# Kernel tuning notes

Measured on AMD Instinct MI355X. Metric: run time of the kernel, lower is better.

## Reference

```python
import jax, jax.numpy as jnp
import numpy as np

EPS_ATTN = 1e-6
LN_EPS = 1e-5

def _layernorm(x, g, b):
    mu = jnp.mean(x, axis=-1, keepdims=True)
    var = jnp.var(x, axis=-1, keepdims=True)
    return (x - mu) * jax.lax.rsqrt(var + LN_EPS) * g + b

def _phi(x):
    return jax.nn.elu(x) + 1.0

def setup_inputs() -> dict:
    key = jax.random.key(0)
    ks = jax.random.split(key, 8)
    B, T, D, H = 2, 4096, 128, 128  # D = token_dim = d+1, H = hidden_dim
    s = 0.02
    return {
        "tokens": jax.random.normal(ks[0], (B, T, D), dtype=jnp.float32),
        "Wq": jax.random.normal(ks[1], (D, H), dtype=jnp.float32) * s,
        "Wk": jax.random.normal(ks[2], (D, H), dtype=jnp.float32) * s,
        "Wv": jax.random.normal(ks[3], (D, D), dtype=jnp.float32) * s,
        "Wg": jax.random.normal(ks[4], (D, D), dtype=jnp.float32) * s,
        "bg": jnp.zeros((D,), dtype=jnp.float32),
        "Wo": jax.random.normal(ks[5], (D, D), dtype=jnp.float32) * s,
        "g1": jnp.ones((D,), dtype=jnp.float32),
        "b1": jnp.zeros((D,), dtype=jnp.float32),
        "g2": jnp.ones((D,), dtype=jnp.float32),
        "b2": jnp.zeros((D,), dtype=jnp.float32),
    }

def reference(tokens, Wq, Wk, Wv, Wg, bg, Wo, g1, b1, g2, b2):
    x = _layernorm(tokens, g1, b1)                 # (b,t,m)
    Q = x @ Wq                                     # (b,t,h)
    K = x @ Wk                                     # (b,t,h)
    V = x @ Wv                                     # (b,t,m)
    G = jax.nn.sigmoid(x @ Wg + bg)                # (b,t,m)
    Vg = V * G
    Qp = _phi(Q)
    Kp = _phi(K)
    # causal linear attention via cumulative outer products
    kv = jnp.einsum('bth,btm->bthm', Kp, Vg)       # (b,t,h,m)
    S_kv = jnp.cumsum(kv, axis=1)
    S_k = jnp.cumsum(Kp, axis=1)
    numerator = jnp.einsum('bth,bthm->btm', Qp, S_kv)
    denom = jnp.maximum(jnp.einsum('bth,bth->bt', Qp, S_k), EPS_ATTN)
    attn_out = numerator / denom[..., None]
    out = tokens + (attn_out @ Wo) * 0.1
    return _layernorm(out, g2, b2)
```

## Files before the change

### kernel.cpp

```cpp
#include <hip/hip_runtime.h>
#include <math.h>

#define T_ 4096
#define D_ 128
#define NTOK 8192
#define CHUNK 64
#define NCB 64
#define NCH 128
#define LN_EPS 1e-5f
#define EPS_ATTN 1e-6f

typedef __attribute__((ext_vector_type(8))) short bf16x8;
typedef __attribute__((ext_vector_type(4))) short bf16x4;
typedef __attribute__((ext_vector_type(4))) float f32x4;

__device__ inline short f2bf(float f) {
  unsigned u = __builtin_bit_cast(unsigned, f);
  u += 0x7fffu + ((u >> 16) & 1u);
  return (short)(u >> 16);
}
__device__ inline float bf2f(short s) {
  unsigned u = ((unsigned)(unsigned short)s) << 16;
  return __builtin_bit_cast(float, u);
}
__device__ inline float phi_(float x) { return x > 0.f ? x + 1.f : __expf(x); }

__global__ __launch_bounds__(256) void k_qkvg(const float* __restrict__ tokens,
    const float* __restrict__ Wq, const float* __restrict__ Wk,
    const float* __restrict__ Wv, const float* __restrict__ Wg,
    const float* __restrict__ g1, const float* __restrict__ b1,
    const float* __restrict__ bg,
    short* __restrict__ Qp, short* __restrict__ Kp, short* __restrict__ KpT,
    short* __restrict__ VgT) {
  const int m0 = blockIdx.x * 64;
  const int y = blockIdx.y;
  const int tid = threadIdx.x;
  const int w = tid >> 6, l = tid & 63;
  __shared__ short xs[64][136];
  __shared__ short wsd[128][136];

  {
    const int half = l >> 5;
    const int c4 = (l & 31) * 4;
    float4 tv[8];
    #pragma unroll
    for (int it = 0; it < 8; ++it) {
      const int t = m0 + w*16 + it*2 + half;
      tv[it] = *(const float4*)&tokens[t*D_ + c4];
    }
    const float4 gg = *(const float4*)&g1[c4];
    const float4 bb = *(const float4*)&b1[c4];
    #pragma unroll
    for (int it = 0; it < 8; ++it) {
      const float4 v = tv[it];
      float s = v.x+v.y+v.z+v.w;
      float q = v.x*v.x+v.y*v.y+v.z*v.z+v.w*v.w;
      #pragma unroll
      for (int off = 1; off < 32; off <<= 1) {
        s += __shfl_xor(s, off); q += __shfl_xor(q, off);
      }
      const float mean = s*(1.f/D_);
      const float r = rsqrtf(q*(1.f/D_) - mean*mean + LN_EPS);
      bf16x4 o;
      o.x = f2bf((v.x-mean)*r*gg.x + bb.x);
      o.y = f2bf((v.y-mean)*r*gg.y + bb.y);
      o.z = f2bf((v.z-mean)*r*gg.z + bb.z);
      o.w = f2bf((v.w-mean)*r*gg.w + bb.w);
      *(bf16x4*)&xs[w*16 + it*2 + half][c4] = o;
    }
  }

  auto stageW = [&](const float* __restrict__ W) {
    #pragma unroll
    for (int it = 0; it < 16; ++it) {
      const int f = it*1024 + tid*4;
      const int k = f >> 7, n = f & 127;
      const float4 v = *(const float4*)&W[f];
      wsd[n  ][k] = f2bf(v.x);
      wsd[n+1][k] = f2bf(v.y);
      wsd[n+2][k] = f2bf(v.z);
      wsd[n+3][k] = f2bf(v.w);
    }
  };

  const int i = l & 15, q = l >> 4;
  auto gemm = [&](f32x4 (*acc)[2]) {
    #pragma unroll
    for (int kk = 0; kk < 4; ++kk) {
      bf16x8 a[4], bfr[2];
      #pragma unroll
      for (int mt = 0; mt < 4; ++mt) a[mt] = *(const bf16x8*)&xs[mt*16+i][kk*32+q*8];
      #pragma unroll
      for (int nt = 0; nt < 2; ++nt) bfr[nt] = *(const bf16x8*)&wsd[w*32+nt*16+i][kk*32+q*8];
      #pragma unroll
      for (int mt = 0; mt < 4; ++mt)
        #pragma unroll
        for (int nt = 0; nt < 2; ++nt)
          acc[mt][nt] = __builtin_amdgcn_mfma_f32_16x16x32_bf16(a[mt], bfr[nt], acc[mt][nt], 0, 0, 0);
    }
  };

  stageW(y == 0 ? Wq : (y == 1 ? Wk : Wv));
  __syncthreads();
  f32x4 acc[4][2];
  #pragma unroll
  for (int mt = 0; mt < 4; ++mt)
    #pragma unroll
    for (int nt = 0; nt < 2; ++nt) acc[mt][nt] = (f32x4){0.f,0.f,0.f,0.f};
  gemm(acc);

  if (y == 0) {
    #pragma unroll
    for (int mt = 0; mt < 4; ++mt)
      #pragma unroll
      for (int nt = 0; nt < 2; ++nt) {
        const int h = w*32 + nt*16 + i;
        #pragma unroll
        for (int r = 0; r < 4; ++r)
          Qp[(m0 + mt*16 + 4*q + r)*D_ + h] = f2bf(phi_(acc[mt][nt][r]));
      }
  } else if (y == 1) {
    #pragma unroll
    for (int mt = 0; mt < 4; ++mt)
      #pragma unroll
      for (int nt = 0; nt < 2; ++nt) {
        const int h = w*32 + nt*16 + i;
        const int t0 = m0 + mt*16 + 4*q;
        bf16x4 o;
        #pragma unroll
        for (int r = 0; r < 4; ++r) {
          const short bv = f2bf(phi_(acc[mt][nt][r]));
          Kp[(t0+r)*D_ + h] = bv;
          o[r] = bv;
        }
        *(bf16x4*)&KpT[h*NTOK + t0] = o;
      }
  } else {
    __syncthreads();
    stageW(Wg);
    __syncthreads();
    f32x4 accg[4][2];
    #pragma unroll
    for (int mt = 0; mt < 4; ++mt)
      #pragma unroll
      for (int nt = 0; nt < 2; ++nt) accg[mt][nt] = (f32x4){0.f,0.f,0.f,0.f};
    gemm(accg);
    #pragma unroll
    for (int mt = 0; mt < 4; ++mt)
      #pragma unroll
      for (int nt = 0; nt < 2; ++nt) {
        const int h = w*32 + nt*16 + i;
        const int t0 = m0 + mt*16 + 4*q;
        const float bgd = bg[h];
        bf16x4 o;
        #pragma unroll
        for (int r = 0; r < 4; ++r) {
          const float gv = 1.f/(1.f + __expf(-(accg[mt][nt][r] + bgd)));
          o[r] = f2bf(acc[mt][nt][r] * gv);
        }
        *(bf16x4*)&VgT[h*NTOK + t0] = o;
      }
  }
}

__global__ __launch_bounds__(256) void k_chunkkv(const short* __restrict__ KpT,
    const short* __restrict__ VgT,
    float* __restrict__ KVT, float* __restrict__ Ksum) {
  const int c = blockIdx.x, hh = blockIdx.y;
  const int tid = threadIdx.x;
  const int tb = c*CHUNK;
  __shared__ short vgl[128][72];
  __shared__ short kpl[64][72];
  __shared__ float ksp[64][5];
  #pragma unroll
  for (int u = tid; u < 1024; u += 256) {
    const int d = u >> 3, c8 = (u & 7)*8;
    *(bf16x8*)&vgl[d][c8] = *(const bf16x8*)&VgT[d*NTOK + tb + c8];
  }
  #pragma unroll
  for (int u = tid; u < 512; u += 256) {
    const int h = u >> 3, c8 = (u & 7)*8;
    *(bf16x8*)&kpl[h][c8] = *(const bf16x8*)&KpT[(hh*64+h)*NTOK + tb + c8];
  }
  __syncthreads();
  const int w = tid >> 6, l = tid & 63, i = l & 15, q = l >> 4;
  f32x4 acc[2][4];
  #pragma unroll
  for (int mt = 0; mt < 2; ++mt)
    #pragma unroll
    for (int nt = 0; nt < 4; ++nt) acc[mt][nt] = (f32x4){0.f,0.f,0.f,0.f};
  #pragma unroll
  for (int kk = 0; kk < 2; ++kk) {
    bf16x8 a[2], bb[4];
    #pragma unroll
    for (int mt = 0; mt < 2; ++mt) a[mt] = *(const bf16x8*)&vgl[(2*w+mt)*16+i][kk*32+q*8];
    #pragma unroll
    for (int nt = 0; nt < 4; ++nt) bb[nt] = *(const bf16x8*)&kpl[nt*16+i][kk*32+q*8];
    #pragma unroll
    for (int mt = 0; mt < 2; ++mt)
      #pragma unroll
      for (int nt = 0; nt < 4; ++nt)
        acc[mt][nt] = __builtin_amdgcn_mfma_f32_16x16x32_bf16(a[mt], bb[nt], acc[mt][nt], 0, 0, 0);
  }
  float* KVc = KVT + (size_t)c*16384;
  #pragma unroll
  for (int mt = 0; mt < 2; ++mt)
    #pragma unroll
    for (int nt = 0; nt < 4; ++nt)
      #pragma unroll
      for (int r = 0; r < 4; ++r) {
        const int d = (2*w+mt)*16 + 4*q + r;
        const int h = hh*64 + nt*16 + i;
        KVc[d*128 + h] = acc[mt][nt][r];
      }
  {
    const int h = tid >> 2, part = tid & 3;
    float s = 0.f;
    #pragma unroll
    for (int t = 0; t < 16; ++t) s += bf2f(kpl[h][part*16 + t]);
    ksp[h][part] = s;
  }
  __syncthreads();
  if (tid < 64)
    Ksum[c*128 + hh*64 + tid] = ksp[tid][0]+ksp[tid][1]+ksp[tid][2]+ksp[tid][3];
}

__global__ __launch_bounds__(256) void k_prescore(const float* __restrict__ KVT,
    short* __restrict__ KVTb, float* __restrict__ Ksum,
    const short* __restrict__ Qp, const short* __restrict__ Kp,
    short* __restrict__ A, float* __restrict__ rowsum) {
  const int tid = threadIdx.x;
  if (blockIdx.x < 128) {
    const int b = blockIdx.x >> 6;
    const int e = (blockIdx.x & 63)*256 + tid;
    const size_t base = (size_t)b*NCB*16384 + e;
    float run = 0.f;
    #pragma unroll 8
    for (int c = 0; c < NCB; ++c) {
      const float v = KVT[base + (size_t)c*16384];
      KVTb[base + (size_t)c*16384] = f2bf(run);
      run += v;
    }
    return;
  }
  if (blockIdx.x == 128) {
    const int b = tid >> 7, h = tid & 127;
    float run = 0.f;
    #pragma unroll 8
    for (int c = 0; c < NCB; ++c) {
      const int idx = (b*NCB + c)*128 + h;
      const float v = Ksum[idx];
      Ksum[idx] = run;
      run += v;
    }
    return;
  }
  const int c = blockIdx.x - 129;
  const int tb = c*CHUNK;
  __shared__ short qpl[64][136], kpl[64][136];
  #pragma unroll
  for (int u = tid; u < 1024; u += 256) {
    const int t = u >> 4, c8 = (u & 15)*8;
    *(bf16x8*)&qpl[t][c8] = *(const bf16x8*)&Qp[(tb+t)*D_ + c8];
    *(bf16x8*)&kpl[t][c8] = *(const bf16x8*)&Kp[(tb+t)*D_ + c8];
  }
  __syncthreads();
  const int w = tid >> 6, l = tid & 63, i = l & 15, q = l >> 4;
  f32x4 acc[4];
  #pragma unroll
  for (int nt = 0; nt < 4; ++nt) acc[nt] = (f32x4){0.f,0.f,0.f,0.f};
  #pragma unroll
  for (int kk = 0; kk < 4; ++kk) {
    bf16x8 a = *(const bf16x8*)&qpl[w*16+i][kk*32+q*8];
    for (int nt = 0; nt <= w; ++nt) {
      bf16x8 bb = *(const bf16x8*)&kpl[nt*16+i][kk*32+q*8];
      acc[nt] = __builtin_amdgcn_mfma_f32_16x16x32_bf16(a, bb, acc[nt], 0, 0, 0);
    }
  }
  short* Ac = A + c*4096;
  float rs[4] = {0.f,0.f,0.f,0.f};
  #pragma unroll
  for (int nt = 0; nt < 4; ++nt) {
    #pragma unroll
    for (int r = 0; r < 4; ++r) {
      const int t = w*16 + 4*q + r;
      const int s = nt*16 + i;
      const float v = (nt <= w && s <= t) ? acc[nt][r] : 0.f;
      rs[r] += v;
      Ac[t*64 + s] = f2bf(v);
    }
  }
  #pragma unroll
  for (int r = 0; r < 4; ++r) {
    #pragma unroll
    for (int off = 1; off < 16; off <<= 1) rs[r] += __shfl_xor(rs[r], off);
  }
  if (i == 0) {
    #pragma unroll
    for (int r = 0; r < 4; ++r) rowsum[c*64 + w*16 + 4*q + r] = rs[r];
  }
}

__global__ __launch_bounds__(256) void k_attnout(const short* __restrict__ Aintra,
    const short* __restrict__ Qp, const short* __restrict__ VgT,
    const short* __restrict__ KVTb, const float* __restrict__ Ksum,
    const float* __restrict__ rowsum, short* __restrict__ attn) {
  const int c = blockIdx.x, dh = blockIdx.y, tid = threadIdx.x;
  const int tb = c*CHUNK;
  __shared__ short at[64][200], bt[64][200];
  __shared__ float ksl[128], dpart[64][4], denl[64];
  const short* Ac = Aintra + c*4096;
  #pragma unroll
  for (int u = tid; u < 512; u += 256) {
    const int t = u >> 3, c8 = (u & 7)*8;
    *(bf16x8*)&at[t][c8] = *(const bf16x8*)&Ac[t*64 + c8];
  }
  #pragma unroll
  for (int u = tid; u < 1024; u += 256) {
    const int t = u >> 4, c8 = (u & 15)*8;
    *(bf16x8*)&at[t][64 + c8] = *(const bf16x8*)&Qp[(tb+t)*D_ + c8];
  }
  #pragma unroll
  for (int u = tid; u < 512; u += 256) {
    const int dd = u >> 3, c8 = (u & 7)*8;
    *(bf16x8*)&bt[dd][c8] = *(const bf16x8*)&VgT[(dh*64+dd)*NTOK + tb + c8];
  }
  #pragma unroll
  for (int u = tid; u < 1024; u += 256) {
    const int dd = u >> 4, c8 = (u & 15)*8;
    *(bf16x8*)&bt[dd][64 + c8] = *(const bf16x8*)&KVTb[(size_t)c*16384 + (dh*64+dd)*128 + c8];
  }
  if (tid < 128) ksl[tid] = Ksum[c*128 + tid];
  __syncthreads();
  {
    const int t = tid >> 2, part = tid & 3;
    float dot = 0.f;
    #pragma unroll
    for (int h = 0; h < 32; ++h) dot += bf2f(at[t][64 + part*32 + h]) * ksl[part*32 + h];
    dpart[t][part] = dot;
  }
  __syncthreads();
  if (tid < 64)
    denl[tid] = fmaxf(rowsum[c*64 + tid] + dpart[tid][0]+dpart[tid][1]+dpart[tid][2]+dpart[tid][3], EPS_ATTN);
  __syncthreads();
  const int w = tid >> 6, l = tid & 63, i = l & 15, q = l >> 4;
  f32x4 acc[4];
  #pragma unroll
  for (int nt = 0; nt < 4; ++nt) acc[nt] = (f32x4){0.f,0.f,0.f,0.f};
  #pragma unroll
  for (int kk = 0; kk < 6; ++kk) {
    bf16x8 a = *(const bf16x8*)&at[w*16+i][kk*32+q*8];
    #pragma unroll
    for (int nt = 0; nt < 4; ++nt) {
      bf16x8 bb = *(const bf16x8*)&bt[nt*16+i][kk*32+q*8];
      acc[nt] = __builtin_amdgcn_mfma_f32_16x16x32_bf16(a, bb, acc[nt], 0, 0, 0);
    }
  }
  #pragma unroll
  for (int r = 0; r < 4; ++r) {
    const int t = w*16 + 4*q + r;
    const float inv = 1.f / denl[t];
    #pragma unroll
    for (int nt = 0; nt < 4; ++nt)
      attn[(size_t)(tb+t)*D_ + dh*64 + nt*16 + i] = f2bf(acc[nt][r] * inv);
  }
}

__global__ __launch_bounds__(256) void k_outln2(const short* __restrict__ attn,
    const float* __restrict__ Wo, const float* __restrict__ tokens,
    const float* __restrict__ g2, const float* __restrict__ b2,
    float* __restrict__ out) {
  const int m0 = blockIdx.x*32, tid = threadIdx.x;
  __shared__ short al[32][136], wl[128][136];
  __shared__ float tl[32][132];
  __shared__ float suml[32][2], ssql[32][2];
  __shared__ float meanl[32], rstdl[32];
  __shared__ float gl[128], bl2[128];
  #pragma unroll
  for (int u = tid; u < 512; u += 256) {
    const int t = u >> 4, c8 = (u & 15)*8;
    *(bf16x8*)&al[t][c8] = *(const bf16x8*)&attn[(m0+t)*D_ + c8];
  }
  #pragma unroll
  for (int it = 0; it < 16; ++it) {
    const int f = it*1024 + tid*4;
    const int k = f >> 7, n = f & 127;
    const float4 v = *(const float4*)&Wo[f];
    wl[n  ][k] = f2bf(v.x);
    wl[n+1][k] = f2bf(v.y);
    wl[n+2][k] = f2bf(v.z);
    wl[n+3][k] = f2bf(v.w);
  }
  #pragma unroll
  for (int u = tid; u < 1024; u += 256) {
    const int t = u >> 5, c4 = (u & 31)*4;
    *(float4*)&tl[t][c4] = *(const float4*)&tokens[(m0+t)*D_ + c4];
  }
  if (tid < 128) { gl[tid] = g2[tid]; bl2[tid] = b2[tid]; }
  __syncthreads();
  const int w = tid >> 6, l = tid & 63, i = l & 15, q = l >> 4;
  const int mt = w >> 1, nh = w & 1;
  f32x4 acc[4];
  #pragma unroll
  for (int j = 0; j < 4; ++j) acc[j] = (f32x4){0.f,0.f,0.f,0.f};
  #pragma unroll
  for (int kk = 0; kk < 4; ++kk) {
    bf16x8 a = *(const bf16x8*)&al[mt*16+i][kk*32+q*8];
    #pragma unroll
    for (int j = 0; j < 4; ++j) {
      bf16x8 bb = *(const bf16x8*)&wl[(nh*4+j)*16+i][kk*32+q*8];
      acc[j] = __builtin_amdgcn_mfma_f32_16x16x32_bf16(a, bb, acc[j], 0, 0, 0);
    }
  }
  float p[4][4], ps[4], qs[4];
  #pragma unroll
  for (int r = 0; r < 4; ++r) {
    const int t = mt*16 + 4*q + r;
    ps[r] = 0.f; qs[r] = 0.f;
    #pragma unroll
    for (int j = 0; j < 4; ++j) {
      const int col = nh*64 + j*16 + i;
      const float v = tl[t][col] + 0.1f*acc[j][r];
      p[r][j] = v; ps[r] += v; qs[r] += v*v;
    }
  }
  #pragma unroll
  for (int r = 0; r < 4; ++r) {
    #pragma unroll
    for (int off = 1; off < 16; off <<= 1) {
      ps[r] += __shfl_xor(ps[r], off);
      qs[r] += __shfl_xor(qs[r], off);
    }
  }
  if (i == 0) {
    #pragma unroll
    for (int r = 0; r < 4; ++r) {
      suml[mt*16+4*q+r][nh] = ps[r];
      ssql[mt*16+4*q+r][nh] = qs[r];
    }
  }
  __syncthreads();
  if (tid < 32) {
    const float s = suml[tid][0] + suml[tid][1];
    const float qq = ssql[tid][0] + ssql[tid][1];
    const float mean = s*(1.f/D_);
    meanl[tid] = mean;
    rstdl[tid] = rsqrtf(qq*(1.f/D_) - mean*mean + LN_EPS);
  }
  __syncthreads();
  #pragma unroll
  for (int r = 0; r < 4; ++r) {
    const int t = mt*16 + 4*q + r;
    const float mean = meanl[t], rr = rstdl[t];
    #pragma unroll
    for (int j = 0; j < 4; ++j) {
      const int col = nh*64 + j*16 + i;
      out[(m0+t)*D_ + col] = (p[r][j]-mean)*rr*gl[col] + bl2[col];
    }
  }
}

extern "C" void kernel_launch(void* const* d_in, const int* in_sizes, int n_in,
                              void* d_out, int out_size, void* d_ws, size_t ws_size,
                              hipStream_t stream) {
  const float* tokens = (const float*)d_in[0];
  const float* Wq = (const float*)d_in[1];
  const float* Wk = (const float*)d_in[2];
  const float* Wv = (const float*)d_in[3];
  const float* Wg = (const float*)d_in[4];
  const float* bg = (const float*)d_in[5];
  const float* Wo = (const float*)d_in[6];
  const float* g1 = (const float*)d_in[7];
  const float* b1 = (const float*)d_in[8];
  const float* g2 = (const float*)d_in[9];
  const float* b2 = (const float*)d_in[10];

  char* base = (char*)d_ws;
  short* Qp     = (short*)(base);
  short* Kp     = (short*)(base + (2u<<20));
  short* KpT    = (short*)(base + (4u<<20));
  short* VgT    = (short*)(base + (6u<<20));
  short* attn   = (short*)(base + (8u<<20));
  short* KVTb   = (short*)(base + (10u<<20));
  short* Aintra = (short*)(base + (14u<<20));
  float* rowsum = (float*)(base + (15u<<20));
  float* Ksum   = (float*)(base + (15u<<20) + (256u<<10));
  float* KVT    = (float*)(base + (16u<<20));

  k_qkvg<<<dim3(NTOK/64, 3), 256, 0, stream>>>(tokens, Wq, Wk, Wv, Wg, g1, b1, bg,
                                               Qp, Kp, KpT, VgT);
  k_chunkkv<<<dim3(NCH, 2), 256, 0, stream>>>(KpT, VgT, KVT, Ksum);
  k_prescore<<<257, 256, 0, stream>>>(KVT, KVTb, Ksum, Qp, Kp, Aintra, rowsum);
  k_attnout<<<dim3(NCH, 2), 256, 0, stream>>>(Aintra, Qp, VgT, KVTb, Ksum, rowsum, attn);
  k_outln2<<<NTOK/32, 256, 0, stream>>>(attn, Wo, tokens, g2, b2, (float*)d_out);
}
```

Measured before the change: 120.3 us.

## Fuse pipeline into persistent megakernel with grid barriers

Replaces the five separate kernel launches with one persistent kernel of 256 blocks that runs each stage in a grid-stride loop, separated by atomic-counter grid barriers. It also pre-transposes and converts the weights to bf16 once, and materializes the layernormed input in bf16. The scan and prescore stages are reorganized, so the chunk-prefix pass and the intra-chunk scoring now run as separate barrier phases. The aim is to remove launch gaps and redundant per-block weight conversion, at the cost of spin-wait barriers, a memset launch, and reliance on all 256 blocks being co-resident.

```diff
diff --git a/kernel.cpp b/kernel.cpp
--- a/kernel.cpp
+++ b/kernel.cpp
@@ -7,6 +7,7 @@
 #define CHUNK 64
 #define NCB 64
 #define NCH 128
+#define NBLK 256
 #define LN_EPS 1e-5f
 #define EPS_ATTN 1e-6f
 
@@ -25,437 +26,463 @@
 }
 __device__ inline float phi_(float x) { return x > 0.f ? x + 1.f : __expf(x); }
 
-__global__ __launch_bounds__(256) void k_qkvg(const float* __restrict__ tokens,
-    const float* __restrict__ Wq, const float* __restrict__ Wk,
-    const float* __restrict__ Wv, const float* __restrict__ Wg,
-    const float* __restrict__ g1, const float* __restrict__ b1,
-    const float* __restrict__ bg,
-    short* __restrict__ Qp, short* __restrict__ Kp, short* __restrict__ KpT,
-    short* __restrict__ VgT) {
-  const int m0 = blockIdx.x * 64;
-  const int y = blockIdx.y;
+__device__ inline void gbar(unsigned* cnt) {
+  __syncthreads();
+  if (threadIdx.x == 0) {
+    __threadfence();
+    atomicAdd(cnt, 1u);
+    while (atomicAdd(cnt, 0u) < NBLK) __builtin_amdgcn_s_sleep(1);
+    __threadfence();
+  }
+  __syncthreads();
+}
+
+struct Params {
+  const float *tokens, *Wq, *Wk, *Wv, *Wg, *bg, *Wo, *g1, *b1, *g2, *b2;
+  short *xb, *WT, *Qp, *Kp, *KpT, *VgT, *attn, *KVTb;
+  float *KVT, *Ksum, *out;
+  unsigned *bar;
+};
+
+struct S0 { float tile[32][33]; };
+struct S1 { short xs[64][136]; short wsd[128][136]; };
+struct S2 { short vgl[128][72]; short kpl[64][72]; float ksp[64][5]; };
+struct S4 { short at[64][200]; short bt[64][200];
+            float ksl[128]; float rsl[64]; float dpart[64][4]; float denl[64]; };
+struct S5 { short al[32][136]; short wl[128][136]; float tl[32][132];
+            float suml[32][2]; float ssql[32][2]; float meanl[32]; float rstdl[32];
+            float gl[128]; float bl2[128]; };
+
+__global__ __launch_bounds__(256, 1) void mega(Params P) {
+  __shared__ union { S0 s0; S1 s1; S2 s2; S4 s4; S5 s5; } sm;
   const int tid = threadIdx.x;
-  const int w = tid >> 6, l = tid & 63;
-  __shared__ short xs[64][136];
-  __shared__ short wsd[128][136];
-
-  {
-    const int half = l >> 5;
-    const int c4 = (l & 31) * 4;
-    float4 tv[8];
-    #pragma unroll
-    for (int it = 0; it < 8; ++it) {
-      const int t = m0 + w*16 + it*2 + half;
-      tv[it] = *(const float4*)&tokens[t*D_ + c4];
-    }
-    const float4 gg = *(const float4*)&g1[c4];
-    const float4 bb = *(const float4*)&b1[c4];
-    #pragma unroll
-    for (int it = 0; it < 8; ++it) {
-      const float4 v = tv[it];
-      float s = v.x+v.y+v.z+v.w;
-      float q = v.x*v.x+v.y*v.y+v.z*v.z+v.w*v.w;
-      #pragma unroll
-      for (int off = 1; off < 32; off <<= 1) {
-        s += __shfl_xor(s, off); q += __shfl_xor(q, off);
-      }
-      const float mean = s*(1.f/D_);
-      const float r = rsqrtf(q*(1.f/D_) - mean*mean + LN_EPS);
-      bf16x4 o;
-      o.x = f2bf((v.x-mean)*r*gg.x + bb.x);
-      o.y = f2bf((v.y-mean)*r*gg.y + bb.y);
-      o.z = f2bf((v.z-mean)*r*gg.z + bb.z);
-      o.w = f2bf((v.w-mean)*r*gg.w + bb.w);
-      *(bf16x4*)&xs[w*16 + it*2 + half][c4] = o;
-    }
-  }
-
-  auto stageW = [&](const float* __restrict__ W) {
-    #pragma unroll
-    for (int it = 0; it < 16; ++it) {
-      const int f = it*1024 + tid*4;
-      const int k = f >> 7, n = f & 127;
-      const float4 v = *(const float4*)&W[f];
-      wsd[n  ][k] = f2bf(v.x);
-      wsd[n+1][k] = f2bf(v.y);
-      wsd[n+2][k] = f2bf(v.z);
-      wsd[n+3][k] = f2bf(v.w);
-    }
-  };
-
-  const int i = l & 15, q = l >> 4;
-  auto gemm = [&](f32x4 (*acc)[2]) {
-    #pragma unroll
-    for (int kk = 0; kk < 4; ++kk) {
-      bf16x8 a[4], bfr[2];
-      #pragma unroll
-      for (int mt = 0; mt < 4; ++mt) a[mt] = *(const bf16x8*)&xs[mt*16+i][kk*32+q*8];
-      #pragma unroll
-      for (int nt = 0; nt < 2; ++nt) bfr[nt] = *(const bf16x8*)&wsd[w*32+nt*16+i][kk*32+q*8];
+  const int bid = blockIdx.x;
+  const int gsz = gridDim.x;
+  const int w = tid >> 6, l = tid & 63, i = l & 15, q = l >> 4;
+
+  for (int u = bid; u < 133; u += gsz) {
+    if (u < 5) {
+      const float* W = u==0?P.Wq : u==1?P.Wk : u==2?P.Wv : u==3?P.Wg : P.Wo;
+      short* dst = P.WT + u*16384;
+      const int r = tid >> 3, c4 = (tid & 7)*4;
+      for (int tt = 0; tt < 16; ++tt) {
+        const int k0 = (tt >> 2)*32, n0 = (tt & 3)*32;
+        __syncthreads();
+        const float4 v = *(const float4*)&W[(k0 + r)*D_ + n0 + c4];
+        sm.s0.tile[r][c4] = v.x; sm.s0.tile[r][c4+1] = v.y;
+        sm.s0.tile[r][c4+2] = v.z; sm.s0.tile[r][c4+3] = v.w;
+        __syncthreads();
+        bf16x4 o;
+        o.x = f2bf(sm.s0.tile[c4+0][r]); o.y = f2bf(sm.s0.tile[c4+1][r]);
+        o.z = f2bf(sm.s0.tile[c4+2][r]); o.w = f2bf(sm.s0.tile[c4+3][r]);
+        *(bf16x4*)&dst[(n0 + r)*D_ + k0 + c4] = o;
+      }
+    } else {
+      const int t0 = (u - 5)*64;
+      const int half = l >> 5;
+      const int c4 = (l & 31)*4;
+      const float4 gg = *(const float4*)&P.g1[c4];
+      const float4 bb = *(const float4*)&P.b1[c4];
+      #pragma unroll
+      for (int it = 0; it < 8; ++it) {
+        const int t = t0 + w*16 + it*2 + half;
+        const float4 v = *(const float4*)&P.tokens[t*D_ + c4];
+        float s = v.x+v.y+v.z+v.w;
+        float qq = v.x*v.x+v.y*v.y+v.z*v.z+v.w*v.w;
+        #pragma unroll
+        for (int off = 1; off < 32; off <<= 1) {
+          s += __shfl_xor(s, off); qq += __shfl_xor(qq, off);
+        }
+        const float mean = s*(1.f/D_);
+        const float r2 = rsqrtf(qq*(1.f/D_) - mean*mean + LN_EPS);
+        bf16x4 o;
+        o.x = f2bf((v.x-mean)*r2*gg.x + bb.x);
+        o.y = f2bf((v.y-mean)*r2*gg.y + bb.y);
+        o.z = f2bf((v.z-mean)*r2*gg.z + bb.z);
+        o.w = f2bf((v.w-mean)*r2*gg.w + bb.w);
+        *(bf16x4*)&P.xb[t*D_ + c4] = o;
+      }
+    }
+  }
+  gbar(P.bar + 0);
+
+  for (int u = bid; u < 256; u += gsz) {
+    if (u < 128) {
+      const int y = u >> 6, p = u & 63;
+      const short* Wb = P.WT + y*16384;
+      for (int v = tid; v < 2048; v += 256) {
+        const int n = v >> 4, c8 = (v & 15)*8;
+        *(bf16x8*)&sm.s1.wsd[n][c8] = *(const bf16x8*)&Wb[n*D_ + c8];
+      }
+      for (int half = 0; half < 2; ++half) {
+        const int m0 = (p*2 + half)*64;
+        __syncthreads();
+        for (int v = tid; v < 1024; v += 256) {
+          const int r = v >> 4, c8 = (v & 15)*8;
+          *(bf16x8*)&sm.s1.xs[r][c8] = *(const bf16x8*)&P.xb[(m0+r)*D_ + c8];
+        }
+        __syncthreads();
+        f32x4 acc[4][2];
+        #pragma unroll
+        for (int mt = 0; mt < 4; ++mt)
+          #pragma unroll
+          for (int nt = 0; nt < 2; ++nt) acc[mt][nt] = (f32x4){0.f,0.f,0.f,0.f};
+        #pragma unroll
+        for (int kk = 0; kk < 4; ++kk) {
+          bf16x8 a[4], bfr[2];
+          #pragma unroll
+          for (int mt = 0; mt < 4; ++mt) a[mt] = *(const bf16x8*)&sm.s1.xs[mt*16+i][kk*32+q*8];
+          #pragma unroll
+          for (int nt = 0; nt < 2; ++nt) bfr[nt] = *(const bf16x8*)&sm.s1.wsd[w*32+nt*16+i][kk*32+q*8];
+          #pragma unroll
+          for (int mt = 0; mt < 4; ++mt)
+            #pragma unroll
+            for (int nt = 0; nt < 2; ++nt)
+              acc[mt][nt] = __builtin_amdgcn_mfma_f32_16x16x32_bf16(a[mt], bfr[nt], acc[mt][nt], 0, 0, 0);
+        }
+        if (y == 0) {
+          #pragma unroll
+          for (int mt = 0; mt < 4; ++mt)
+            #pragma unroll
+            for (int nt = 0; nt < 2; ++nt) {
+              const int h = w*32 + nt*16 + i;
+              #pragma unroll
+              for (int r = 0; r < 4; ++r)
+                P.Qp[(m0 + mt*16 + 4*q + r)*D_ + h] = f2bf(phi_(acc[mt][nt][r]));
+            }
+        } else {
+          #pragma unroll
+          for (int mt = 0; mt < 4; ++mt)
+            #pragma unroll
+            for (int nt = 0; nt < 2; ++nt) {
+              const int h = w*32 + nt*16 + i;
+              const int t0 = m0 + mt*16 + 4*q;
+              bf16x4 o;
+              #pragma unroll
+              for (int r = 0; r < 4; ++r) {
+                const short bv = f2bf(phi_(acc[mt][nt][r]));
+                P.Kp[(t0+r)*D_ + h] = bv;
+                o[r] = bv;
+              }
+              *(bf16x4*)&P.KpT[h*NTOK + t0] = o;
+            }
+        }
+      }
+    } else {
+      const int m0 = (u - 128)*64;
+      __syncthreads();
+      for (int v = tid; v < 1024; v += 256) {
+        const int r = v >> 4, c8 = (v & 15)*8;
+        *(bf16x8*)&sm.s1.xs[r][c8] = *(const bf16x8*)&P.xb[(m0+r)*D_ + c8];
+      }
+      const short* Wvb = P.WT + 2*16384;
+      for (int v = tid; v < 2048; v += 256) {
+        const int n = v >> 4, c8 = (v & 15)*8;
+        *(bf16x8*)&sm.s1.wsd[n][c8] = *(const bf16x8*)&Wvb[n*D_ + c8];
+      }
+      __syncthreads();
+      f32x4 accv[4][2], accg[4][2];
       #pragma unroll
       for (int mt = 0; mt < 4; ++mt)
         #pragma unroll
-        for (int nt = 0; nt < 2; ++nt)
-          acc[mt][nt] = __builtin_amdgcn_mfma_f32_16x16x32_bf16(a[mt], bfr[nt], acc[mt][nt], 0, 0, 0);
-    }
-  };
-
-  stageW(y == 0 ? Wq : (y == 1 ? Wk : Wv));
-  __syncthreads();
-  f32x4 acc[4][2];
-  #pragma unroll
-  for (int mt = 0; mt < 4; ++mt)
-    #pragma unroll
-    for (int nt = 0; nt < 2; ++nt) acc[mt][nt] = (f32x4){0.f,0.f,0.f,0.f};
-  gemm(acc);
-
-  if (y == 0) {
-    #pragma unroll
-    for (int mt = 0; mt < 4; ++mt)
-      #pragma unroll
-      for (int nt = 0; nt < 2; ++nt) {
-        const int h = w*32 + nt*16 + i;
+        for (int nt = 0; nt < 2; ++nt) {
+          accv[mt][nt] = (f32x4){0.f,0.f,0.f,0.f};
+          accg[mt][nt] = (f32x4){0.f,0.f,0.f,0.f};
+        }
+      #pragma unroll
+      for (int kk = 0; kk < 4; ++kk) {
+        bf16x8 a[4], bfr[2];
+        #pragma unroll
+        for (int mt = 0; mt < 4; ++mt) a[mt] = *(const bf16x8*)&sm.s1.xs[mt*16+i][kk*32+q*8];
+        #pragma unroll
+        for (int nt = 0; nt < 2; ++nt) bfr[nt] = *(const bf16x8*)&sm.s1.wsd[w*32+nt*16+i][kk*32+q*8];
+        #pragma unroll
+        for (int mt = 0; mt < 4; ++mt)
+          #pragma unroll
+          for (int nt = 0; nt < 2; ++nt)
+            accv[mt][nt] = __builtin_amdgcn_mfma_f32_16x16x32_bf16(a[mt], bfr[nt], accv[mt][nt], 0, 0, 0);
+      }
+      __syncthreads();
+      const short* Wgb = P.WT + 3*16384;
+      for (int v = tid; v < 2048; v += 256) {
+        const int n = v >> 4, c8 = (v & 15)*8;
+        *(bf16x8*)&sm.s1.wsd[n][c8] = *(const bf16x8*)&Wgb[n*D_ + c8];
+      }
+      __syncthreads();
+      #pragma unroll
+      for (int kk = 0; kk < 4; ++kk) {
+        bf16x8 a[4], bfr[2];
+        #pragma unroll
+        for (int mt = 0; mt < 4; ++mt) a[mt] = *(const bf16x8*)&sm.s1.xs[mt*16+i][kk*32+q*8];
+        #pragma unroll
+        for (int nt = 0; nt < 2; ++nt) bfr[nt] = *(const bf16x8*)&sm.s1.wsd[w*32+nt*16+i][kk*32+q*8];
+        #pragma unroll
+        for (int mt = 0; mt < 4; ++mt)
+          #pragma unroll
+          for (int nt = 0; nt < 2; ++nt)
+            accg[mt][nt] = __builtin_amdgcn_mfma_f32_16x16x32_bf16(a[mt], bfr[nt], accg[mt][nt], 0, 0, 0);
+      }
+      #pragma unroll
+      for (int mt = 0; mt < 4; ++mt)
+        #pragma unroll
+        for (int nt = 0; nt < 2; ++nt) {
+          const int h = w*32 + nt*16 + i;
+          const int t0 = m0 + mt*16 + 4*q;
+          const float bgd = P.bg[h];
+          bf16x4 o;
+          #pragma unroll
+          for (int r = 0; r < 4; ++r) {
+            const float gv = 1.f/(1.f + __expf(-(accg[mt][nt][r] + bgd)));
+            o[r] = f2bf(accv[mt][nt][r] * gv);
+          }
+          *(bf16x4*)&P.VgT[h*NTOK + t0] = o;
+        }
+    }
+  }
+  gbar(P.bar + 1);
+
+  for (int u = bid; u < 256; u += gsz) {
+    const int c = u >> 1, hh = u & 1;
+    const int tb = c*CHUNK;
+    __syncthreads();
+    for (int v = tid; v < 1024; v += 256) {
+      const int d = v >> 3, c8 = (v & 7)*8;
+      *(bf16x8*)&sm.s2.vgl[d][c8] = *(const bf16x8*)&P.VgT[d*NTOK + tb + c8];
+    }
+    for (int v = tid; v < 512; v += 256) {
+      const int h = v >> 3, c8 = (v & 7)*8;
+      *(bf16x8*)&sm.s2.kpl[h][c8] = *(const bf16x8*)&P.KpT[(hh*64+h)*NTOK + tb + c8];
+    }
+    __syncthreads();
+    f32x4 acc[2][4];
+    #pragma unroll
+    for (int mt = 0; mt < 2; ++mt)
+      #pragma unroll
+      for (int nt = 0; nt < 4; ++nt) acc[mt][nt] = (f32x4){0.f,0.f,0.f,0.f};
+    #pragma unroll
+    for (int kk = 0; kk < 2; ++kk) {
+      bf16x8 a[2], bb[4];
+      #pragma unroll
+      for (int mt = 0; mt < 2; ++mt) a[mt] = *(const bf16x8*)&sm.s2.vgl[(2*w+mt)*16+i][kk*32+q*8];
+      #pragma unroll
+      for (int nt = 0; nt < 4; ++nt) bb[nt] = *(const bf16x8*)&sm.s2.kpl[nt*16+i][kk*32+q*8];
+      #pragma unroll
+      for (int mt = 0; mt < 2; ++mt)
+        #pragma unroll
+        for (int nt = 0; nt < 4; ++nt)
+          acc[mt][nt] = __builtin_amdgcn_mfma_f32_16x16x32_bf16(a[mt], bb[nt], acc[mt][nt], 0, 0, 0);
+    }
+    float* KVc = P.KVT + (size_t)c*16384;
+    #pragma unroll
+    for (int mt = 0; mt < 2; ++mt)
+      #pragma unroll
+      for (int nt = 0; nt < 4; ++nt)
         #pragma unroll
         for (int r = 0; r < 4; ++r)
-          Qp[(m0 + mt*16 + 4*q + r)*D_ + h] = f2bf(phi_(acc[mt][nt][r]));
-      }
-  } else if (y == 1) {
-    #pragma unroll
-    for (int mt = 0; mt < 4; ++mt)
-      #pragma unroll
-      for (int nt = 0; nt < 2; ++nt) {
-        const int h = w*32 + nt*16 + i;
-        const int t0 = m0 + mt*16 + 4*q;
-        bf16x4 o;
+          KVc[((2*w+mt)*16 + 4*q + r)*D_ + hh*64 + nt*16 + i] = acc[mt][nt][r];
+    {
+      const int h = tid >> 2, part = tid & 3;
+      float s = 0.f;
+      #pragma unroll
+      for (int t = 0; t < 16; ++t) s += bf2f(sm.s2.kpl[h][part*16 + t]);
+      sm.s2.ksp[h][part] = s;
+    }
+    __syncthreads();
+    if (tid < 64)
+      P.Ksum[c*D_ + hh*64 + tid] = sm.s2.ksp[tid][0]+sm.s2.ksp[tid][1]+sm.s2.ksp[tid][2]+sm.s2.ksp[tid][3];
+  }
+  gbar(P.bar + 2);
+
+  for (int u = bid; u < 129; u += gsz) {
+    if (u < 128) {
+      const int b = u >> 6;
+      const int e = (u & 63)*256 + tid;
+      const size_t base = (size_t)b*NCB*16384 + e;
+      float run = 0.f;
+      #pragma unroll 8
+      for (int c = 0; c < NCB; ++c) {
+        const float v = P.KVT[base + (size_t)c*16384];
+        P.KVTb[base + (size_t)c*16384] = f2bf(run);
+        run += v;
+      }
+    } else {
+      const int b = tid >> 7, h = tid & 127;
+      float run = 0.f;
+      #pragma unroll 8
+      for (int c = 0; c < NCB; ++c) {
+        const int idx = (b*NCB + c)*D_ + h;
+        const float v = P.Ksum[idx];
+        P.Ksum[idx] = run;
+        run += v;
+      }
+    }
+  }
+  gbar(P.bar + 3);
+
+  for (int u = bid; u < 256; u += gsz) {
+    const int c = u >> 1, dh = u & 1;
+    const int tb = c*CHUNK;
+    __syncthreads();
+    for (int v = tid; v < 1024; v += 256) {
+      const int t = v >> 4, c8 = (v & 15)*8;
+      *(bf16x8*)&sm.s4.at[t][64 + c8] = *(const bf16x8*)&P.Qp[(tb+t)*D_ + c8];
+      *(bf16x8*)&sm.s4.bt[t][c8]      = *(const bf16x8*)&P.Kp[(tb+t)*D_ + c8];
+    }
+    if (tid < 128) sm.s4.ksl[tid] = P.Ksum[c*D_ + tid];
+    __syncthreads();
+    {
+      f32x4 acc[4];
+      #pragma unroll
+      for (int nt = 0; nt < 4; ++nt) acc[nt] = (f32x4){0.f,0.f,0.f,0.f};
+      #pragma unroll
+      for (int kk = 0; kk < 4; ++kk) {
+        bf16x8 a = *(const bf16x8*)&sm.s4.at[w*16+i][64 + kk*32+q*8];
+        for (int nt = 0; nt <= w; ++nt) {
+          bf16x8 bb = *(const bf16x8*)&sm.s4.bt[nt*16+i][kk*32+q*8];
+          acc[nt] = __builtin_amdgcn_mfma_f32_16x16x32_bf16(a, bb, acc[nt], 0, 0, 0);
+        }
+      }
+      float rs[4] = {0.f,0.f,0.f,0.f};
+      #pragma unroll
+      for (int nt = 0; nt < 4; ++nt)
         #pragma unroll
         for (int r = 0; r < 4; ++r) {
-          const short bv = f2bf(phi_(acc[mt][nt][r]));
-          Kp[(t0+r)*D_ + h] = bv;
-          o[r] = bv;
-        }
-        *(bf16x4*)&KpT[h*NTOK + t0] = o;
-      }
-  } else {
-    __syncthreads();
-    stageW(Wg);
-    __syncthreads();
-    f32x4 accg[4][2];
-    #pragma unroll
-    for (int mt = 0; mt < 4; ++mt)
-      #pragma unroll
-      for (int nt = 0; nt < 2; ++nt) accg[mt][nt] = (f32x4){0.f,0.f,0.f,0.f};
-    gemm(accg);
-    #pragma unroll
-    for (int mt = 0; mt < 4; ++mt)
-      #pragma unroll
-      for (int nt = 0; nt < 2; ++nt) {
-        const int h = w*32 + nt*16 + i;
-        const int t0 = m0 + mt*16 + 4*q;
-        const float bgd = bg[h];
-        bf16x4 o;
-        #pragma unroll
-        for (int r = 0; r < 4; ++r) {
-          const float gv = 1.f/(1.f + __expf(-(accg[mt][nt][r] + bgd)));
-          o[r] = f2bf(acc[mt][nt][r] * gv);
-        }
-        *(bf16x4*)&VgT[h*NTOK + t0] = o;
-      }
-  }
-}
-
-__global__ __launch_bounds__(256) void k_chunkkv(const short* __restrict__ KpT,
-    const short* __restrict__ VgT,
-    float* __restrict__ KVT, float* __restrict__ Ksum) {
-  const int c = blockIdx.x, hh = blockIdx.y;
-  const int tid = threadIdx.x;
-  const int tb = c*CHUNK;
-  __shared__ short vgl[128][72];
-  __shared__ short kpl[64][72];
-  __shared__ float ksp[64][5];
-  #pragma unroll
-  for (int u = tid; u < 1024; u += 256) {
-    const int d = u >> 3, c8 = (u & 7)*8;
-    *(bf16x8*)&vgl[d][c8] = *(const bf16x8*)&VgT[d*NTOK + tb + c8];
-  }
-  #pragma unroll
-  for (int u = tid; u < 512; u += 256) {
-    const int h = u >> 3, c8 = (u & 7)*8;
-    *(bf16x8*)&kpl[h][c8] = *(const bf16x8*)&KpT[(hh*64+h)*NTOK + tb + c8];
-  }
-  __syncthreads();
-  const int w = tid >> 6, l = tid & 63, i = l & 15, q = l >> 4;
-  f32x4 acc[2][4];
-  #pragma unroll
-  for (int mt = 0; mt < 2; ++mt)
-    #pragma unroll
-    for (int nt = 0; nt < 4; ++nt) acc[mt][nt] = (f32x4){0.f,0.f,0.f,0.f};
-  #pragma unroll
-  for (int kk = 0; kk < 2; ++kk) {
-    bf16x8 a[2], bb[4];
-    #pragma unroll
-    for (int mt = 0; mt < 2; ++mt) a[mt] = *(const bf16x8*)&vgl[(2*w+mt)*16+i][kk*32+q*8];
-    #pragma unroll
-    for (int nt = 0; nt < 4; ++nt) bb[nt] = *(const bf16x8*)&kpl[nt*16+i][kk*32+q*8];
-    #pragma unroll
-    for (int mt = 0; mt < 2; ++mt)
-      #pragma unroll
-      for (int nt = 0; nt < 4; ++nt)
-        acc[mt][nt] = __builtin_amdgcn_mfma_f32_16x16x32_bf16(a[mt], bb[nt], acc[mt][nt], 0, 0, 0);
-  }
-  float* KVc = KVT + (size_t)c*16384;
-  #pragma unroll
-  for (int mt = 0; mt < 2; ++mt)
-    #pragma unroll
-    for (int nt = 0; nt < 4; ++nt)
+          const int t = w*16 + 4*q + r;
+          const int s = nt*16 + i;
+          const float v = (nt <= w && s <= t) ? acc[nt][r] : 0.f;
+          rs[r] += v;
+          sm.s4.at[t][s] = f2bf(v);
+        }
       #pragma unroll
       for (int r = 0; r < 4; ++r) {
-        const int d = (2*w+mt)*16 + 4*q + r;
-        const int h = hh*64 + nt*16 + i;
-        KVc[d*128 + h] = acc[mt][nt][r];
-      }
-  {
-    const int h = tid >> 2, part = tid & 3;
-    float s = 0.f;
-    #pragma unroll
-    for (int t = 0; t < 16; ++t) s += bf2f(kpl[h][part*16 + t]);
-    ksp[h][part] = s;
-  }
-  __syncthreads();
-  if (tid < 64)
-    Ksum[c*128 + hh*64 + tid] = ksp[tid][0]+ksp[tid][1]+ksp[tid][2]+ksp[tid][3];
-}
-
-__global__ __launch_bounds__(256) void k_prescore(const float* __restrict__ KVT,
-    short* __restrict__ KVTb, float* __restrict__ Ksum,
-    const short* __restrict__ Qp, const short* __restrict__ Kp,
-    short* __restrict__ A, float* __restrict__ rowsum) {
-  const int tid = threadIdx.x;
-  if (blockIdx.x < 128) {
-    const int b = blockIdx.x >> 6;
-    const int e = (blockIdx.x & 63)*256 + tid;
-    const size_t base = (size_t)b*NCB*16384 + e;
-    float run = 0.f;
-    #pragma unroll 8
-    for (int c = 0; c < NCB; ++c) {
-      const float v = KVT[base + (size_t)c*16384];
-      KVTb[base + (size_t)c*16384] = f2bf(run);
-      run += v;
-    }
-    return;
-  }
-  if (blockIdx.x == 128) {
-    const int b = tid >> 7, h = tid & 127;
-    float run = 0.f;
-    #pragma unroll 8
-    for (int c = 0; c < NCB; ++c) {
-      const int idx = (b*NCB + c)*128 + h;
-      const float v = Ksum[idx];
-      Ksum[idx] = run;
-      run += v;
-    }
-    return;
-  }
-  const int c = blockIdx.x - 129;
-  const int tb = c*CHUNK;
-  __shared__ short qpl[64][136], kpl[64][136];
-  #pragma unroll
-  for (int u = tid; u < 1024; u += 256) {
-    const int t = u >> 4, c8 = (u & 15)*8;
-    *(bf16x8*)&qpl[t][c8] = *(const bf16x8*)&Qp[(tb+t)*D_ + c8];
-    *(bf16x8*)&kpl[t][c8] = *(const bf16x8*)&Kp[(tb+t)*D_ + c8];
-  }
-  __syncthreads();
-  const int w = tid >> 6, l = tid & 63, i = l & 15, q = l >> 4;
-  f32x4 acc[4];
-  #pragma unroll
-  for (int nt = 0; nt < 4; ++nt) acc[nt] = (f32x4){0.f,0.f,0.f,0.f};
-  #pragma unroll
-  for (int kk = 0; kk < 4; ++kk) {
-    bf16x8 a = *(const bf16x8*)&qpl[w*16+i][kk*32+q*8];
-    for (int nt = 0; nt <= w; ++nt) {
-      bf16x8 bb = *(const bf16x8*)&kpl[nt*16+i][kk*32+q*8];
-      acc[nt] = __builtin_amdgcn_mfma_f32_16x16x32_bf16(a, bb, acc[nt], 0, 0, 0);
-    }
-  }
-  short* Ac = A + c*4096;
-  float rs[4] = {0.f,0.f,0.f,0.f};
-  #pragma unroll
-  for (int nt = 0; nt < 4; ++nt) {
+        #pragma unroll
+        for (int off = 1; off < 16; off <<= 1) rs[r] += __shfl_xor(rs[r], off);
+      }
+      if (i == 0) {
+        #pragma unroll
+        for (int r = 0; r < 4; ++r) sm.s4.rsl[w*16 + 4*q + r] = rs[r];
+      }
+    }
+    {
+      const int t = tid >> 2, part = tid & 3;
+      float dot = 0.f;
+      #pragma unroll
+      for (int h = 0; h < 32; ++h)
+        dot += bf2f(sm.s4.at[t][64 + part*32 + h]) * sm.s4.ksl[part*32 + h];
+      sm.s4.dpart[t][part] = dot;
+    }
+    __syncthreads();
+    if (tid < 64)
+      sm.s4.denl[tid] = fmaxf(sm.s4.rsl[tid] + sm.s4.dpart[tid][0]+sm.s4.dpart[tid][1]
+                              +sm.s4.dpart[tid][2]+sm.s4.dpart[tid][3], EPS_ATTN);
+    for (int v = tid; v < 512; v += 256) {
+      const int dd = v >> 3, c8 = (v & 7)*8;
+      *(bf16x8*)&sm.s4.bt[dd][c8] = *(const bf16x8*)&P.VgT[(dh*64+dd)*NTOK + tb + c8];
+    }
+    for (int v = tid; v < 1024; v += 256) {
+      const int dd = v >> 4, c8 = (v & 15)*8;
+      *(bf16x8*)&sm.s4.bt[dd][64 + c8] = *(const bf16x8*)&P.KVTb[(size_t)c*16384 + (dh*64+dd)*D_ + c8];
+    }
+    __syncthreads();
+    f32x4 acc2[4];
+    #pragma unroll
+    for (int nt = 0; nt < 4; ++nt) acc2[nt] = (f32x4){0.f,0.f,0.f,0.f};
+    #pragma unroll
+    for (int kk = 0; kk < 6; ++kk) {
+      bf16x8 a = *(const bf16x8*)&sm.s4.at[w*16+i][kk*32+q*8];
+      #pragma unroll
+      for (int nt = 0; nt < 4; ++nt) {
+        bf16x8 bb = *(const bf16x8*)&sm.s4.bt[nt*16+i][kk*32+q*8];
+        acc2[nt] = __builtin_amdgcn_mfma_f32_16x16x32_bf16(a, bb, acc2[nt], 0, 0, 0);
+      }
+    }
     #pragma unroll
     for (int r = 0; r < 4; ++r) {
       const int t = w*16 + 4*q + r;
-      const int s = nt*16 + i;
-      const float v = (nt <= w && s <= t) ? acc[nt][r] : 0.f;
-      rs[r] += v;
-      Ac[t*64 + s] = f2bf(v);
-    }
-  }
-  #pragma unroll
-  for (int r = 0; r < 4; ++r) {
-    #pragma unroll
-    for (int off = 1; off < 16; off <<= 1) rs[r] += __shfl_xor(rs[r], off);
-  }
-  if (i == 0) {
-    #pragma unroll
-    for (int r = 0; r < 4; ++r) rowsum[c*64 + w*16 + 4*q + r] = rs[r];
-  }
-}
-
-__global__ __launch_bounds__(256) void k_attnout(const short* __restrict__ Aintra,
-    const short* __restrict__ Qp, const short* __restrict__ VgT,
-    const short* __restrict__ KVTb, const float* __restrict__ Ksum,
-    const float* __restrict__ rowsum, short* __restrict__ attn) {
-  const int c = blockIdx.x, dh = blockIdx.y, tid = threadIdx.x;
-  const int tb = c*CHUNK;
-  __shared__ short at[64][200], bt[64][200];
-  __shared__ float ksl[128], dpart[64][4], denl[64];
-  const short* Ac = Aintra + c*4096;
-  #pragma unroll
-  for (int u = tid; u < 512; u += 256) {
-    const int t = u >> 3, c8 = (u & 7)*8;
-    *(bf16x8*)&at[t][c8] = *(const bf16x8*)&Ac[t*64 + c8];
-  }
-  #pragma unroll
-  for (int u = tid; u < 1024; u += 256) {
-    const int t = u >> 4, c8 = (u & 15)*8;
-    *(bf16x8*)&at[t][64 + c8] = *(const bf16x8*)&Qp[(tb+t)*D_ + c8];
-  }
-  #pragma unroll
-  for (int u = tid; u < 512; u += 256) {
-    const int dd = u >> 3, c8 = (u & 7)*8;
-    *(bf16x8*)&bt[dd][c8] = *(const bf16x8*)&VgT[(dh*64+dd)*NTOK + tb + c8];
-  }
-  #pragma unroll
-  for (int u = tid; u < 1024; u += 256) {
-    const int dd = u >> 4, c8 = (u & 15)*8;
-    *(bf16x8*)&bt[dd][64 + c8] = *(const bf16x8*)&KVTb[(size_t)c*16384 + (dh*64+dd)*128 + c8];
-  }
-  if (tid < 128) ksl[tid] = Ksum[c*128 + tid];
-  __syncthreads();
-  {
-    const int t = tid >> 2, part = tid & 3;
-    float dot = 0.f;
-    #pragma unroll
-    for (int h = 0; h < 32; ++h) dot += bf2f(at[t][64 + part*32 + h]) * ksl[part*32 + h];
-    dpart[t][part] = dot;
-  }
-  __syncthreads();
-  if (tid < 64)
-    denl[tid] = fmaxf(rowsum[c*64 + tid] + dpart[tid][0]+dpart[tid][1]+dpart[tid][2]+dpart[tid][3], EPS_ATTN);
-  __syncthreads();
-  const int w = tid >> 6, l = tid & 63, i = l & 15, q = l >> 4;
-  f32x4 acc[4];
-  #pragma unroll
-  for (int nt = 0; nt < 4; ++nt) acc[nt] = (f32x4){0.f,0.f,0.f,0.f};
-  #pragma unroll
-  for (int kk = 0; kk < 6; ++kk) {
-    bf16x8 a = *(const bf16x8*)&at[w*16+i][kk*32+q*8];
-    #pragma unroll
-    for (int nt = 0; nt < 4; ++nt) {
-      bf16x8 bb = *(const bf16x8*)&bt[nt*16+i][kk*32+q*8];
-      acc[nt] = __builtin_amdgcn_mfma_f32_16x16x32_bf16(a, bb, acc[nt], 0, 0, 0);
-    }
-  }
-  #pragma unroll
-  for (int r = 0; r < 4; ++r) {
-    const int t = w*16 + 4*q + r;
-    const float inv = 1.f / denl[t];
-    #pragma unroll
-    for (int nt = 0; nt < 4; ++nt)
-      attn[(size_t)(tb+t)*D_ + dh*64 + nt*16 + i] = f2bf(acc[nt][r] * inv);
-  }
-}
-
-__global__ __launch_bounds__(256) void k_outln2(const short* __restrict__ attn,
-    const float* __restrict__ Wo, const float* __restrict__ tokens,
-    const float* __restrict__ g2, const float* __restrict__ b2,
-    float* __restrict__ out) {
-  const int m0 = blockIdx.x*32, tid = threadIdx.x;
-  __shared__ short al[32][136], wl[128][136];
-  __shared__ float tl[32][132];
-  __shared__ float suml[32][2], ssql[32][2];
-  __shared__ float meanl[32], rstdl[32];
-  __shared__ float gl[128], bl2[128];
-  #pragma unroll
-  for (int u = tid; u < 512; u += 256) {
-    const int t = u >> 4, c8 = (u & 15)*8;
-    *(bf16x8*)&al[t][c8] = *(const bf16x8*)&attn[(m0+t)*D_ + c8];
-  }
-  #pragma unroll
-  for (int it = 0; it < 16; ++it) {
-    const int f = it*1024 + tid*4;
-    const int k = f >> 7, n = f & 127;
-    const float4 v = *(const float4*)&Wo[f];
-    wl[n  ][k] = f2bf(v.x);
-    wl[n+1][k] = f2bf(v.y);
-    wl[n+2][k] = f2bf(v.z);
-    wl[n+3][k] = f2bf(v.w);
-  }
-  #pragma unroll
-  for (int u = tid; u < 1024; u += 256) {
-    const int t = u >> 5, c4 = (u & 31)*4;
-    *(float4*)&tl[t][c4] = *(const float4*)&tokens[(m0+t)*D_ + c4];
-  }
-  if (tid < 128) { gl[tid] = g2[tid]; bl2[tid] = b2[tid]; }
-  __syncthreads();
-  const int w = tid >> 6, l = tid & 63, i = l & 15, q = l >> 4;
-  const int mt = w >> 1, nh = w & 1;
-  f32x4 acc[4];
-  #pragma unroll
-  for (int j = 0; j < 4; ++j) acc[j] = (f32x4){0.f,0.f,0.f,0.f};
-  #pragma unroll
-  for (int kk = 0; kk < 4; ++kk) {
-    bf16x8 a = *(const bf16x8*)&al[mt*16+i][kk*32+q*8];
-    #pragma unroll
-    for (int j = 0; j < 4; ++j) {
-      bf16x8 bb = *(const bf16x8*)&wl[(nh*4+j)*16+i][kk*32+q*8];
-      acc[j] = __builtin_amdgcn_mfma_f32_16x16x32_bf16(a, bb, acc[j], 0, 0, 0);
-    }
-  }
-  float p[4][4], ps[4], qs[4];
-  #pragma unroll
-  for (int r = 0; r < 4; ++r) {
-    const int t = mt*16 + 4*q + r;
-    ps[r] = 0.f; qs[r] = 0.f;
-    #pragma unroll
-    for (int j = 0; j < 4; ++j) {
-      const int col = nh*64 + j*16 + i;
-      const float v = tl[t][col] + 0.1f*acc[j][r];
-      p[r][j] = v; ps[r] += v; qs[r] += v*v;
-    }
-  }
-  #pragma unroll
-  for (int r = 0; r < 4; ++r) {
-    #pragma unroll
-    for (int off = 1; off < 16; off <<= 1) {
-      ps[r] += __shfl_xor(ps[r], off);
-      qs[r] += __shfl_xor(qs[r], off);
-    }
-  }
-  if (i == 0) {
+      const float inv = 1.f / sm.s4.denl[t];
+      #pragma unroll
+      for (int nt = 0; nt < 4; ++nt)
+        P.attn[(size_t)(tb+t)*D_ + dh*64 + nt*16 + i] = f2bf(acc2[nt][r] * inv);
+    }
+  }
+  gbar(P.bar + 4);
+
+  for (int u = bid; u < 256; u += gsz) {
+    const int m0 = u*32;
+    __syncthreads();
+    for (int v = tid; v < 512; v += 256) {
+      const int t = v >> 4, c8 = (v & 15)*8;
+      *(bf16x8*)&sm.s5.al[t][c8] = *(const bf16x8*)&P.attn[(m0+t)*D_ + c8];
+    }
+    const short* WoT = P.WT + 4*16384;
+    for (int v = tid; v < 2048; v += 256) {
+      const int n = v >> 4, c8 = (v & 15)*8;
+      *(bf16x8*)&sm.s5.wl[n][c8] = *(const bf16x8*)&WoT[n*D_ + c8];
+    }
+    for (int v = tid; v < 1024; v += 256) {
+      const int t = v >> 5, c4 = (v & 31)*4;
+      *(float4*)&sm.s5.tl[t][c4] = *(const float4*)&P.tokens[(m0+t)*D_ + c4];
+    }
+    if (tid < 128) { sm.s5.gl[tid] = P.g2[tid]; sm.s5.bl2[tid] = P.b2[tid]; }
+    __syncthreads();
+    const int mt = w >> 1, nh = w & 1;
+    f32x4 acc[4];
+    #pragma unroll
+    for (int j = 0; j < 4; ++j) acc[j] = (f32x4){0.f,0.f,0.f,0.f};
+    #pragma unroll
+    for (int kk = 0; kk < 4; ++kk) {
+      bf16x8 a = *(const bf16x8*)&sm.s5.al[mt*16+i][kk*32+q*8];
+      #pragma unroll
+      for (int j = 0; j < 4; ++j) {
+        bf16x8 bb = *(const bf16x8*)&sm.s5.wl[(nh*4+j)*16+i][kk*32+q*8];
+        acc[j] = __builtin_amdgcn_mfma_f32_16x16x32_bf16(a, bb, acc[j], 0, 0, 0);
+      }
+    }
+    float p[4][4], ps[4], qs[4];
     #pragma unroll
     for (int r = 0; r < 4; ++r) {
-      suml[mt*16+4*q+r][nh] = ps[r];
-      ssql[mt*16+4*q+r][nh] = qs[r];
-    }
-  }
-  __syncthreads();
-  if (tid < 32) {
-    const float s = suml[tid][0] + suml[tid][1];
-    const float qq = ssql[tid][0] + ssql[tid][1];
-    const float mean = s*(1.f/D_);
-    meanl[tid] = mean;
-    rstdl[tid] = rsqrtf(qq*(1.f/D_) - mean*mean + LN_EPS);
-  }
-  __syncthreads();
-  #pragma unroll
-  for (int r = 0; r < 4; ++r) {
-    const int t = mt*16 + 4*q + r;
-    const float mean = meanl[t], rr = rstdl[t];
-    #pragma unroll
-    for (int j = 0; j < 4; ++j) {
-      const int col = nh*64 + j*16 + i;
-      out[(m0+t)*D_ + col] = (p[r][j]-mean)*rr*gl[col] + bl2[col];
+      const int t = mt*16 + 4*q + r;
+      ps[r] = 0.f; qs[r] = 0.f;
+      #pragma unroll
+      for (int j = 0; j < 4; ++j) {
+        const int col = nh*64 + j*16 + i;
+        const float v = sm.s5.tl[t][col] + 0.1f*acc[j][r];
+        p[r][j] = v; ps[r] += v; qs[r] += v*v;
+      }
+    }
+    #pragma unroll
+    for (int r = 0; r < 4; ++r) {
+      #pragma unroll
+      for (int off = 1; off < 16; off <<= 1) {
+        ps[r] += __shfl_xor(ps[r], off);
+        qs[r] += __shfl_xor(qs[r], off);
+      }
+    }
+    if (i == 0) {
+      #pragma unroll
+      for (int r = 0; r < 4; ++r) {
+        sm.s5.suml[mt*16+4*q+r][nh] = ps[r];
+        sm.s5.ssql[mt*16+4*q+r][nh] = qs[r];
+      }
+    }
+    __syncthreads();
+    if (tid < 32) {
+      const float s = sm.s5.suml[tid][0] + sm.s5.suml[tid][1];
+      const float qq = sm.s5.ssql[tid][0] + sm.s5.ssql[tid][1];
+      const float mean = s*(1.f/D_);
+      sm.s5.meanl[tid] = mean;
+      sm.s5.rstdl[tid] = rsqrtf(qq*(1.f/D_) - mean*mean + LN_EPS);
+    }
+    __syncthreads();
+    #pragma unroll
+    for (int r = 0; r < 4; ++r) {
+      const int t = mt*16 + 4*q + r;
+      const float mean = sm.s5.meanl[t], rr = sm.s5.rstdl[t];
+      #pragma unroll
+      for (int j = 0; j < 4; ++j) {
+        const int col = nh*64 + j*16 + i;
+        P.out[(m0+t)*D_ + col] = (p[r][j]-mean)*rr*sm.s5.gl[col] + sm.s5.bl2[col];
+      }
     }
   }
 }
@@ -463,34 +490,27 @@
 extern "C" void kernel_launch(void* const* d_in, const int* in_sizes, int n_in,
                               void* d_out, int out_size, void* d_ws, size_t ws_size,
                               hipStream_t stream) {
-  const float* tokens = (const float*)d_in[0];
-  const float* Wq = (const float*)d_in[1];
-  const float* Wk = (const float*)d_in[2];
-  const float* Wv = (const float*)d_in[3];
-  const float* Wg = (const float*)d_in[4];
-  const float* bg = (const float*)d_in[5];
-  const float* Wo = (const float*)d_in[6];
-  const float* g1 = (const float*)d_in[7];
-  const float* b1 = (const float*)d_in[8];
-  const float* g2 = (const float*)d_in[9];
-  const float* b2 = (const float*)d_in[10];
-
   char* base = (char*)d_ws;
-  short* Qp     = (short*)(base);
-  short* Kp     = (short*)(base + (2u<<20));
-  short* KpT    = (short*)(base + (4u<<20));
-  short* VgT    = (short*)(base + (6u<<20));
-  short* attn   = (short*)(base + (8u<<20));
-  short* KVTb   = (short*)(base + (10u<<20));
-  short* Aintra = (short*)(base + (14u<<20));
-  float* rowsum = (float*)(base + (15u<<20));
-  float* Ksum   = (float*)(base + (15u<<20) + (256u<<10));
-  float* KVT    = (float*)(base + (16u<<20));
-
-  k_qkvg<<<dim3(NTOK/64, 3), 256, 0, stream>>>(tokens, Wq, Wk, Wv, Wg, g1, b1, bg,
-                                               Qp, Kp, KpT, VgT);
-  k_chunkkv<<<dim3(NCH, 2), 256, 0, stream>>>(KpT, VgT, KVT, Ksum);
-  k_prescore<<<257, 256, 0, stream>>>(KVT, KVTb, Ksum, Qp, Kp, Aintra, rowsum);
-  k_attnout<<<dim3(NCH, 2), 256, 0, stream>>>(Aintra, Qp, VgT, KVTb, Ksum, rowsum, attn);
-  k_outln2<<<NTOK/32, 256, 0, stream>>>(attn, Wo, tokens, g2, b2, (float*)d_out);
+  Params P;
+  P.tokens = (const float*)d_in[0];
+  P.Wq = (const float*)d_in[1];  P.Wk = (const float*)d_in[2];
+  P.Wv = (const float*)d_in[3];  P.Wg = (const float*)d_in[4];
+  P.bg = (const float*)d_in[5];  P.Wo = (const float*)d_in[6];
+  P.g1 = (const float*)d_in[7];  P.b1 = (const float*)d_in[8];
+  P.g2 = (const float*)d_in[9];  P.b2 = (const float*)d_in[10];
+  P.xb   = (short*)(base);
+  P.Qp   = (short*)(base + (2u<<20));
+  P.Kp   = (short*)(base + (4u<<20));
+  P.KpT  = (short*)(base + (6u<<20));
+  P.VgT  = (short*)(base + (8u<<20));
+  P.attn = (short*)(base + (10u<<20));
+  P.KVTb = (short*)(base + (12u<<20));
+  P.KVT  = (float*)(base + (16u<<20));
+  P.WT   = (short*)(base + (24u<<20));
+  P.Ksum = (float*)(base + (25u<<20));
+  P.bar  = (unsigned*)(base + (25u<<20) + (128u<<10));
+  P.out  = (float*)d_out;
+
+  hipMemsetAsync(P.bar, 0, 8*sizeof(unsigned), stream);
+  mega<<<dim3(NBLK), dim3(256), 0, stream>>>(P);
 }
```

Result: slower. 232.0 us (+92.9%).
